# Kernel tuning notes

Hardware: AMD Instinct MI355X
Metric: run time of the kernel (lower is better)

## Reference

```python
import jax, jax.numpy as jnp
import numpy as np

N_NODES = 50000
N_EDGES = 800000
F_IN, H, C1, C2 = 256, 128, 4, 3


def gcn_conv(x, W, b, src, dst, n_nodes):
    # PyG GCNConv: add self-loops, symmetric normalization D^-1/2 A D^-1/2,
    # linear transform, scatter-add aggregation at dst, then bias.
    loop = jnp.arange(n_nodes, dtype=src.dtype)
    s = jnp.concatenate([src, loop])
    d = jnp.concatenate([dst, loop])
    deg = jax.ops.segment_sum(jnp.ones_like(d, dtype=x.dtype), d, num_segments=n_nodes)
    dinv = jnp.where(deg > 0, jax.lax.rsqrt(deg), 0.0)
    norm = dinv[s] * dinv[d]                      # [E+N]
    h = x @ W                                     # [N, out]
    msg = h[s] * norm[:, None]                    # gather + scale
    out = jax.ops.segment_sum(msg, d, num_segments=n_nodes)  # scatter-add
    return out + b


def setup_inputs() -> dict:
    key = jax.random.key(0)
    ks = jax.random.split(key, 10)
    x = jax.random.normal(ks[0], (N_NODES, F_IN), dtype=jnp.float32)
    edge_index = jax.random.randint(ks[1], (2, N_EDGES), 0, N_NODES, dtype=jnp.int32)
    def lin(k, fan_in, fan_out):
        bound = 1.0 / np.sqrt(fan_in)
        kw, kb = jax.random.split(k)
        W = jax.random.uniform(kw, (fan_in, fan_out), jnp.float32, -bound, bound)
        b = jax.random.uniform(kb, (fan_out,), jnp.float32, -bound, bound)
        return W, b
    W1, b1 = lin(ks[2], F_IN, H)
    W2, b2 = lin(ks[3], H, H)
    Wh1, bh1 = lin(ks[4], H, C1)
    Wh2, bh2 = lin(ks[5], H, C2)
    return {"x": x, "edge_index": edge_index, "W1": W1, "b1": b1,
            "W2": W2, "b2": b2, "Wh1": Wh1, "bh1": bh1, "Wh2": Wh2, "bh2": bh2}


def reference(x, edge_index, W1, b1, W2, b2, Wh1, bh1, Wh2, bh2):
    # Eval-mode forward (dropout p=0.5 is identity at inference; l2_classifier=False).
    src, dst = edge_index[0], edge_index[1]
    h = gcn_conv(x, W1, b1, src, dst, N_NODES)
    h = jax.nn.relu(h)
    h = gcn_conv(h, W2, b2, src, dst, N_NODES)
    out1 = h @ Wh1 + bh1
    out2 = h @ Wh2 + bh2
    return (out1, out2, h)
```

## Files before the change

### kernel.cpp

```cpp
#include <hip/hip_runtime.h>

#define NN 50000
#define NE 800000
#define FIN 256
#define HD 128
#define CAP 96

typedef unsigned int uint;
typedef unsigned short ushort;

__device__ inline ushort f2bf(float f) {
    uint u = __float_as_uint(f);
    u += 0x7fffu + ((u >> 16) & 1u);
    return (ushort)(u >> 16);
}
__device__ inline void unpack2(uint u, float& a, float& b) {
    a = __uint_as_float(u << 16);
    b = __uint_as_float(u & 0xffff0000u);
}


__global__ void build_buckets(const int* __restrict__ ei, int* __restrict__ cnt,
                              int* __restrict__ bucket) {
    int e = blockIdx.x * 256 + threadIdx.x;
    if (e >= NE) return;
    int s = ei[e];
    int d = ei[NE + e];
    int pos = atomicAdd(&cnt[d], 1);
    if (pos < CAP) bucket[d * CAP + pos] = s;
}

__global__ void compute_dinv(const int* __restrict__ cnt, float* __restrict__ dinv) {
    int v = blockIdx.x * 256 + threadIdx.x;
    if (v < NN) dinv[v] = rsqrtf((float)cnt[v] + 1.0f);
}


template<int K>
__global__ __launch_bounds__(256) void gemm_n128(const float* __restrict__ A,
                                                 const float* __restrict__ B,
                                                 const float* __restrict__ dscale,
                                                 ushort* __restrict__ C, int M) {
    __shared__ float As[16][64];
    __shared__ float Bs[16][128];
    const int tid = threadIdx.x;
    const int tx = tid & 15;
    const int ty = tid >> 4;
    const int blockRow = blockIdx.x * 64;

    float acc[4][8];
#pragma unroll
    for (int r = 0; r < 4; ++r)
#pragma unroll
        for (int j = 0; j < 8; ++j) acc[r][j] = 0.f;

    const int la_row = tid >> 2;
    const int la_k   = (tid & 3) << 2;
    const int lb_k   = tid >> 5;
    const int lb_col = (tid & 31) << 2;
    const int arow   = blockRow + la_row;

    for (int k0 = 0; k0 < K; k0 += 16) {
        float4 av = make_float4(0.f, 0.f, 0.f, 0.f);
        if (arow < M) av = *(const float4*)(A + (size_t)arow * K + k0 + la_k);
        As[la_k + 0][la_row] = av.x;
        As[la_k + 1][la_row] = av.y;
        As[la_k + 2][la_row] = av.z;
        As[la_k + 3][la_row] = av.w;
        *(float4*)&Bs[lb_k][lb_col]     = *(const float4*)(B + (size_t)(k0 + lb_k) * 128 + lb_col);
        *(float4*)&Bs[lb_k + 8][lb_col] = *(const float4*)(B + (size_t)(k0 + lb_k + 8) * 128 + lb_col);
        __syncthreads();
#pragma unroll
        for (int k = 0; k < 16; ++k) {
            float4 a  = *(const float4*)&As[k][ty << 2];
            float4 b0 = *(const float4*)&Bs[k][tx << 2];
            float4 b1 = *(const float4*)&Bs[k][64 + (tx << 2)];
            const float aa[4] = {a.x, a.y, a.z, a.w};
            const float bb[8] = {b0.x, b0.y, b0.z, b0.w, b1.x, b1.y, b1.z, b1.w};
#pragma unroll
            for (int r = 0; r < 4; ++r)
#pragma unroll
                for (int j = 0; j < 8; ++j)
                    acc[r][j] = fmaf(aa[r], bb[j], acc[r][j]);
        }
        __syncthreads();
    }

#pragma unroll
    for (int r = 0; r < 4; ++r) {
        int row = blockRow + (ty << 2) + r;
        if (row < M) {
            float ds = dscale[row];
            uint2 w0, w1;
            w0.x = (uint)f2bf(ds * acc[r][0]) | ((uint)f2bf(ds * acc[r][1]) << 16);
            w0.y = (uint)f2bf(ds * acc[r][2]) | ((uint)f2bf(ds * acc[r][3]) << 16);
            w1.x = (uint)f2bf(ds * acc[r][4]) | ((uint)f2bf(ds * acc[r][5]) << 16);
            w1.y = (uint)f2bf(ds * acc[r][6]) | ((uint)f2bf(ds * acc[r][7]) << 16);
            *(uint2*)(C + (size_t)row * 128 + (tx << 2))      = w0;
            *(uint2*)(C + (size_t)row * 128 + 64 + (tx << 2)) = w1;
        }
    }
}


template<int RELU, int HEADS>
__global__ __launch_bounds__(256) void aggregate(const ushort* __restrict__ hb,
                                                 const int* __restrict__ cnt,
                                                 const int* __restrict__ bucket,
                                                 const float* __restrict__ dinv,
                                                 const float* __restrict__ bias,
                                                 float* __restrict__ out,
                                                 const float* __restrict__ Wh1,
                                                 const float* __restrict__ bh1,
                                                 const float* __restrict__ Wh2,
                                                 const float* __restrict__ bh2,
                                                 float* __restrict__ out1,
                                                 float* __restrict__ out2) {
    int v = (blockIdx.x << 2) + (threadIdx.x >> 6);
    if (v >= NN) return;
    const int lane = threadIdx.x & 63;
    const int g = lane >> 4;
    const int q = lane & 15;
    int c = cnt[v]; if (c > CAP) c = CAP;
    const int total = c + 1;
    const float di = dinv[v];
    const int* bk = bucket + (size_t)v * CAP;

    float acc[8];
#pragma unroll
    for (int j = 0; j < 8; ++j) acc[j] = 0.f;

    auto slotof = [&](int k) -> int {
        return k < c ? bk[k] : (k == c ? v : NN);
    };
    auto rowload = [&](int s) -> uint4 {
        return *(const uint4*)(hb + (size_t)s * 128 + (q << 3));
    };

    int sA = slotof(g);
    int sB = slotof(4 + g);
    uint4 rA = rowload(sA);
    uint4 rB = rowload(sB);
    int sC = slotof(8 + g);
    int sD = slotof(12 + g);

    for (int e = 0; e < total; e += 8) {
        uint4 rA2 = rowload(sC);
        uint4 rB2 = rowload(sD);
        sC = slotof(e + 16 + g);
        sD = slotof(e + 20 + g);
        float f0, f1, f2, f3, f4, f5, f6, f7;
        unpack2(rA.x, f0, f1); unpack2(rA.y, f2, f3);
        unpack2(rA.z, f4, f5); unpack2(rA.w, f6, f7);
        acc[0] += f0; acc[1] += f1; acc[2] += f2; acc[3] += f3;
        acc[4] += f4; acc[5] += f5; acc[6] += f6; acc[7] += f7;
        unpack2(rB.x, f0, f1); unpack2(rB.y, f2, f3);
        unpack2(rB.z, f4, f5); unpack2(rB.w, f6, f7);
        acc[0] += f0; acc[1] += f1; acc[2] += f2; acc[3] += f3;
        acc[4] += f4; acc[5] += f5; acc[6] += f6; acc[7] += f7;
        rA = rA2; rB = rB2;
    }

#pragma unroll
    for (int j = 0; j < 8; ++j) {
        acc[j] += __shfl_xor(acc[j], 16);
        acc[j] += __shfl_xor(acc[j], 32);
    }

    float4 bb0 = *(const float4*)(bias + (q << 3));
    float4 bb1 = *(const float4*)(bias + (q << 3) + 4);
    float o[8];
    o[0] = fmaf(di, acc[0], bb0.x); o[1] = fmaf(di, acc[1], bb0.y);
    o[2] = fmaf(di, acc[2], bb0.z); o[3] = fmaf(di, acc[3], bb0.w);
    o[4] = fmaf(di, acc[4], bb1.x); o[5] = fmaf(di, acc[5], bb1.y);
    o[6] = fmaf(di, acc[6], bb1.z); o[7] = fmaf(di, acc[7], bb1.w);
    if (RELU) {
#pragma unroll
        for (int j = 0; j < 8; ++j) o[j] = fmaxf(o[j], 0.f);
    }

    if (g < 2) {
        int j0 = (g & 1) << 2;
        *(float4*)(out + (size_t)v * 128 + (q << 3) + j0) =
            make_float4(o[j0], o[j0 + 1], o[j0 + 2], o[j0 + 3]);
    }

    if (HEADS) {
        const int kb = q << 3;
        float p[7];
#pragma unroll
        for (int cc = 0; cc < 4; ++cc) {
            float s = 0.f;
#pragma unroll
            for (int j = 0; j < 8; ++j) s = fmaf(o[j], Wh1[(kb + j) * 4 + cc], s);
            p[cc] = s;
        }
#pragma unroll
        for (int cc = 0; cc < 3; ++cc) {
            float s = 0.f;
#pragma unroll
            for (int j = 0; j < 8; ++j) s = fmaf(o[j], Wh2[(kb + j) * 3 + cc], s);
            p[4 + cc] = s;
        }
#pragma unroll
        for (int i = 0; i < 7; ++i) {
            float s = p[i];
            s += __shfl_xor(s, 1);
            s += __shfl_xor(s, 2);
            s += __shfl_xor(s, 4);
            s += __shfl_xor(s, 8);
            p[i] = s;
        }
        if (lane == 0) {
            out1[(size_t)v * 4 + 0] = p[0] + bh1[0];
            out1[(size_t)v * 4 + 1] = p[1] + bh1[1];
            out1[(size_t)v * 4 + 2] = p[2] + bh1[2];
            out1[(size_t)v * 4 + 3] = p[3] + bh1[3];
            out2[(size_t)v * 3 + 0] = p[4] + bh2[0];
            out2[(size_t)v * 3 + 1] = p[5] + bh2[1];
            out2[(size_t)v * 3 + 2] = p[6] + bh2[2];
        }
    }
}


extern "C" void kernel_launch(void* const* d_in, const int* in_sizes, int n_in,
                              void* d_out, int out_size, void* d_ws, size_t ws_size,
                              hipStream_t stream) {
    const float* x   = (const float*)d_in[0];
    const int*   ei  = (const int*)d_in[1];
    const float* W1  = (const float*)d_in[2];
    const float* b1  = (const float*)d_in[3];
    const float* W2  = (const float*)d_in[4];
    const float* b2  = (const float*)d_in[5];
    const float* Wh1 = (const float*)d_in[6];
    const float* bh1 = (const float*)d_in[7];
    const float* Wh2 = (const float*)d_in[8];
    const float* bh2 = (const float*)d_in[9];

    float* out1 = (float*)d_out;
    float* out2 = out1 + (size_t)NN * 4;
    float* hout = out2 + (size_t)NN * 3;

    char* ws = (char*)d_ws;
    auto alloc = [&](size_t bytes) { char* p = ws; ws += (bytes + 255) & ~(size_t)255; return p; };
    int*    cnt    = (int*)   alloc((size_t)NN * 4);
    float*  dinv   = (float*) alloc((size_t)NN * 4);
    int*    bucket = (int*)   alloc((size_t)NN * CAP * 4);
    ushort* hlinb  = (ushort*)alloc((size_t)(NN + 1) * HD * 2);
    float*  hagg   = (float*) alloc((size_t)NN * HD * 4);

    hipMemsetAsync(cnt, 0, (size_t)NN * 4, stream);
    hipMemsetAsync(hlinb + (size_t)NN * HD, 0, HD * 2, stream);
    build_buckets<<<(NE + 255) / 256, 256, 0, stream>>>(ei, cnt, bucket);
    compute_dinv<<<(NN + 255) / 256, 256, 0, stream>>>(cnt, dinv);

    gemm_n128<FIN><<<(NN + 63) / 64, 256, 0, stream>>>(x, W1, dinv, hlinb, NN);
    aggregate<1, 0><<<(NN + 3) / 4, 256, 0, stream>>>(hlinb, cnt, bucket, dinv, b1, hagg,
                                                      nullptr, nullptr, nullptr, nullptr,
                                                      nullptr, nullptr);

    gemm_n128<HD><<<(NN + 63) / 64, 256, 0, stream>>>(hagg, W2, dinv, hlinb, NN);
    aggregate<0, 1><<<(NN + 3) / 4, 256, 0, stream>>>(hlinb, cnt, bucket, dinv, b2, hout,
                                                      Wh1, bh1, Wh2, bh2, out1, out2);
}
```

Baseline: 352.5 us.

## Replace FP32 SIMT GEMM with bf16 MFMA using split-precision activations

Swaps the scalar FMA GEMM for a 16x16x32 bf16 MFMA kernel. Activations are split into high and low bf16 parts to keep near-fp32 accuracy. Weights are pre-transposed and converted to bf16 by a small prep kernel on each call. This aims to cut GEMM compute time, at the cost of two MFMAs per tile, extra conversion work, lower weight precision, and scalar 2-byte output stores.

Measured after the change: 298.2 us. 1.18x faster.

```diff
diff --git a/kernel.cpp b/kernel.cpp
--- a/kernel.cpp
+++ b/kernel.cpp
@@ -8,12 +8,15 @@
 
 typedef unsigned int uint;
 typedef unsigned short ushort;
+typedef __attribute__((ext_vector_type(8))) short short8v;
+typedef __attribute__((ext_vector_type(4))) float f32x4;
 
 __device__ inline ushort f2bf(float f) {
     uint u = __float_as_uint(f);
     u += 0x7fffu + ((u >> 16) & 1u);
     return (ushort)(u >> 16);
 }
+__device__ inline float bf2f(ushort h) { return __uint_as_float(((uint)h) << 16); }
 __device__ inline void unpack2(uint u, float& a, float& b) {
     a = __uint_as_float(u << 16);
     b = __uint_as_float(u & 0xffff0000u);
@@ -37,67 +40,81 @@
 
 
 template<int K>
-__global__ __launch_bounds__(256) void gemm_n128(const float* __restrict__ A,
-                                                 const float* __restrict__ B,
+__global__ void prep_wt(const float* __restrict__ W, ushort* __restrict__ Wt) {
+    int idx = blockIdx.x * 256 + threadIdx.x;
+    if (idx >= K * 128) return;
+    int k = idx >> 7, col = idx & 127;
+    Wt[col * K + k] = f2bf(W[idx]);
+}
+
+
+template<int K>
+__global__ __launch_bounds__(256) void gemm_mfma(const float* __restrict__ A,
+                                                 const ushort* __restrict__ Wt,
                                                  const float* __restrict__ dscale,
                                                  ushort* __restrict__ C, int M) {
-    __shared__ float As[16][64];
-    __shared__ float Bs[16][128];
-    const int tid = threadIdx.x;
-    const int tx = tid & 15;
-    const int ty = tid >> 4;
+    __shared__ ushort Ah[64][40];
+    __shared__ ushort Al[64][40];
+    __shared__ ushort Bt[128][40];
+    const int tid  = threadIdx.x;
+    const int wid  = tid >> 6;
+    const int lane = tid & 63;
+    const int fr   = lane & 15;
+    const int kg   = lane >> 4;
+
     const int blockRow = blockIdx.x * 64;
 
-    float acc[4][8];
-#pragma unroll
-    for (int r = 0; r < 4; ++r)
-#pragma unroll
-        for (int j = 0; j < 8; ++j) acc[r][j] = 0.f;
-
-    const int la_row = tid >> 2;
-    const int la_k   = (tid & 3) << 2;
-    const int lb_k   = tid >> 5;
-    const int lb_col = (tid & 31) << 2;
-    const int arow   = blockRow + la_row;
-
-    for (int k0 = 0; k0 < K; k0 += 16) {
-        float4 av = make_float4(0.f, 0.f, 0.f, 0.f);
-        if (arow < M) av = *(const float4*)(A + (size_t)arow * K + k0 + la_k);
-        As[la_k + 0][la_row] = av.x;
-        As[la_k + 1][la_row] = av.y;
-        As[la_k + 2][la_row] = av.z;
-        As[la_k + 3][la_row] = av.w;
-        *(float4*)&Bs[lb_k][lb_col]     = *(const float4*)(B + (size_t)(k0 + lb_k) * 128 + lb_col);
-        *(float4*)&Bs[lb_k + 8][lb_col] = *(const float4*)(B + (size_t)(k0 + lb_k + 8) * 128 + lb_col);
+    f32x4 acc[8];
+#pragma unroll
+    for (int n = 0; n < 8; ++n) acc[n] = (f32x4){0.f, 0.f, 0.f, 0.f};
+
+    const int s_ar = tid >> 3;
+    const int s_ak = (tid & 7) << 2;
+
+    for (int k0 = 0; k0 < K; k0 += 32) {
+#pragma unroll
+        for (int i = 0; i < 2; ++i) {
+            int r = i * 32 + s_ar;
+            int row = blockRow + r;
+            float4 av = make_float4(0.f, 0.f, 0.f, 0.f);
+            if (row < M) av = *(const float4*)(A + (size_t)row * K + k0 + s_ak);
+            ushort h0 = f2bf(av.x), h1 = f2bf(av.y), h2 = f2bf(av.z), h3 = f2bf(av.w);
+            ushort l0 = f2bf(av.x - bf2f(h0)), l1 = f2bf(av.y - bf2f(h1));
+            ushort l2 = f2bf(av.z - bf2f(h2)), l3 = f2bf(av.w - bf2f(h3));
+            uint2 hw, lw;
+            hw.x = (uint)h0 | ((uint)h1 << 16); hw.y = (uint)h2 | ((uint)h3 << 16);
+            lw.x = (uint)l0 | ((uint)l1 << 16); lw.y = (uint)l2 | ((uint)l3 << 16);
+            *(uint2*)&Ah[r][s_ak] = hw;
+            *(uint2*)&Al[r][s_ak] = lw;
+        }
+#pragma unroll
+        for (int i = 0; i < 2; ++i) {
+            int id = i * 256 + tid;
+            int col = id >> 2;
+            int kc = (id & 3) << 3;
+            *(uint4*)&Bt[col][kc] = *(const uint4*)(Wt + (size_t)col * K + k0 + kc);
+        }
         __syncthreads();
-#pragma unroll
-        for (int k = 0; k < 16; ++k) {
-            float4 a  = *(const float4*)&As[k][ty << 2];
-            float4 b0 = *(const float4*)&Bs[k][tx << 2];
-            float4 b1 = *(const float4*)&Bs[k][64 + (tx << 2)];
-            const float aa[4] = {a.x, a.y, a.z, a.w};
-            const float bb[8] = {b0.x, b0.y, b0.z, b0.w, b1.x, b1.y, b1.z, b1.w};
-#pragma unroll
-            for (int r = 0; r < 4; ++r)
-#pragma unroll
-                for (int j = 0; j < 8; ++j)
-                    acc[r][j] = fmaf(aa[r], bb[j], acc[r][j]);
+        short8v a_h = *(short8v*)&Ah[(wid << 4) + fr][kg << 3];
+        short8v a_l = *(short8v*)&Al[(wid << 4) + fr][kg << 3];
+#pragma unroll
+        for (int n = 0; n < 8; ++n) {
+            short8v b = *(short8v*)&Bt[(n << 4) + fr][kg << 3];
+            acc[n] = __builtin_amdgcn_mfma_f32_16x16x32_bf16(a_h, b, acc[n], 0, 0, 0);
+            acc[n] = __builtin_amdgcn_mfma_f32_16x16x32_bf16(a_l, b, acc[n], 0, 0, 0);
         }
         __syncthreads();
     }
 
+    const int rbase = blockRow + (wid << 4) + (kg << 2);
 #pragma unroll
     for (int r = 0; r < 4; ++r) {
-        int row = blockRow + (ty << 2) + r;
+        int row = rbase + r;
         if (row < M) {
             float ds = dscale[row];
-            uint2 w0, w1;
-            w0.x = (uint)f2bf(ds * acc[r][0]) | ((uint)f2bf(ds * acc[r][1]) << 16);
-            w0.y = (uint)f2bf(ds * acc[r][2]) | ((uint)f2bf(ds * acc[r][3]) << 16);
-            w1.x = (uint)f2bf(ds * acc[r][4]) | ((uint)f2bf(ds * acc[r][5]) << 16);
-            w1.y = (uint)f2bf(ds * acc[r][6]) | ((uint)f2bf(ds * acc[r][7]) << 16);
-            *(uint2*)(C + (size_t)row * 128 + (tx << 2))      = w0;
-            *(uint2*)(C + (size_t)row * 128 + 64 + (tx << 2)) = w1;
+#pragma unroll
+            for (int n = 0; n < 8; ++n)
+                C[(size_t)row * 128 + (n << 4) + fr] = f2bf(ds * acc[n][r]);
         }
     }
 }
@@ -249,18 +266,22 @@
     int*    bucket = (int*)   alloc((size_t)NN * CAP * 4);
     ushort* hlinb  = (ushort*)alloc((size_t)(NN + 1) * HD * 2);
     float*  hagg   = (float*) alloc((size_t)NN * HD * 4);
+    ushort* Wt1    = (ushort*)alloc((size_t)128 * FIN * 2);
+    ushort* Wt2    = (ushort*)alloc((size_t)128 * HD * 2);
 
     hipMemsetAsync(cnt, 0, (size_t)NN * 4, stream);
     hipMemsetAsync(hlinb + (size_t)NN * HD, 0, HD * 2, stream);
     build_buckets<<<(NE + 255) / 256, 256, 0, stream>>>(ei, cnt, bucket);
     compute_dinv<<<(NN + 255) / 256, 256, 0, stream>>>(cnt, dinv);
-
-    gemm_n128<FIN><<<(NN + 63) / 64, 256, 0, stream>>>(x, W1, dinv, hlinb, NN);
+    prep_wt<FIN><<<(FIN * 128 + 255) / 256, 256, 0, stream>>>(W1, Wt1);
+    prep_wt<HD><<<(HD * 128 + 255) / 256, 256, 0, stream>>>(W2, Wt2);
+
+    gemm_mfma<FIN><<<(NN + 63) / 64, 256, 0, stream>>>(x, Wt1, dinv, hlinb, NN);
     aggregate<1, 0><<<(NN + 3) / 4, 256, 0, stream>>>(hlinb, cnt, bucket, dinv, b1, hagg,
                                                       nullptr, nullptr, nullptr, nullptr,
                                                       nullptr, nullptr);
 
-    gemm_n128<HD><<<(NN + 63) / 64, 256, 0, stream>>>(hagg, W2, dinv, hlinb, NN);
+    gemm_mfma<HD><<<(NN + 63) / 64, 256, 0, stream>>>(hagg, Wt2, dinv, hlinb, NN);
     aggregate<0, 1><<<(NN + 3) / 4, 256, 0, stream>>>(hlinb, cnt, bucket, dinv, b2, hout,
                                                       Wh1, bh1, Wh2, bh2, out1, out2);
 }
```
